# Kernel optimization log

Hardware: AMD Instinct MI355X
Metric: run time of the kernel (lower is better)

## Reference

```python
import jax, jax.numpy as jnp
import numpy as np

S, B, I, H = 512, 256, 256, 256


def setup_inputs() -> dict:
    key = jax.random.key(0)
    ks = jax.random.split(key, 8)
    sc = 0.1
    inputs = jax.random.normal(ks[0], (S, B, I), dtype=jnp.float32)
    h0 = jax.random.normal(ks[1], (1, B, H), dtype=jnp.float32)
    c0 = jax.random.normal(ks[2], (1, B, H), dtype=jnp.float32)
    done = jax.random.randint(ks[3], (S, B), 0, 2).astype(jnp.float32)
    W_ih = jax.random.normal(ks[4], (4 * H, I), dtype=jnp.float32) * sc
    W_hh = jax.random.normal(ks[5], (4 * H, H), dtype=jnp.float32) * sc
    b_ih = jax.random.normal(ks[6], (4 * H,), dtype=jnp.float32) * sc
    b_hh = jax.random.normal(ks[7], (4 * H,), dtype=jnp.float32) * sc
    return {"inputs": inputs, "h0": h0, "c0": c0, "done": done,
            "W_ih": W_ih, "W_hh": W_hh, "b_ih": b_ih, "b_hh": b_hh}


def _lstm_with_dones(inputs, h0, c0, done, W_ih, W_hh, b_ih, b_hh):
    Hd = h0.shape[-1]
    bias = b_ih + b_hh  # (4H,)
    # Precompute input projections for all timesteps: (S, B, 4H)
    x_proj = jnp.einsum('sbi,gi->sbg', inputs, W_ih) + bias

    def step(carry, xs):
        h, c = carry                      # (B, H) each
        xp, d = xs                        # (B, 4H), (B,)
        mask = (1.0 - d)[:, None]         # reset state where done
        h = h * mask
        c = c * mask
        gates = xp + h @ W_hh.T           # (B, 4H), torch gate order i,f,g,o
        i_g, f_g, g_g, o_g = jnp.split(gates, 4, axis=-1)
        c = jax.nn.sigmoid(f_g) * c + jax.nn.sigmoid(i_g) * jnp.tanh(g_g)
        h = jax.nn.sigmoid(o_g) * jnp.tanh(c)
        return (h, c), h

    (hT, cT), hs = jax.lax.scan(step, (h0[0], c0[0]), (x_proj, done))
    new_hidden = hs.reshape(-1, Hd)       # flatten (S, B, H) -> (S*B, H)
    return new_hidden, hT[None], cT[None]


def reference(inputs, h0, c0, done, W_ih, W_hh, b_ih, b_hh):
    return _lstm_with_dones(inputs, h0, c0, done, W_ih, W_hh, b_ih, b_hh)
```

## Files before the change

### kernel.cpp

```cpp
#include <hip/hip_runtime.h>
#include <hip/hip_bf16.h>

typedef unsigned int u32;
typedef unsigned short u16;
typedef __attribute__((ext_vector_type(8))) short bf16x8;
typedef __attribute__((ext_vector_type(8))) unsigned short u16x8;
typedef __attribute__((ext_vector_type(4))) float f32x4;
typedef __attribute__((ext_vector_type(4))) float f4;

#define HS_TOTAL 33554432
#define MAXTILES 2048


__device__ __forceinline__ u16 f2bf(float f) {
  u32 u = __builtin_bit_cast(u32, f);
  u += 0x7fffu + ((u >> 16) & 1u);
  return (u16)(u >> 16);
}
__device__ __forceinline__ float sigm(float x) {
  return __builtin_amdgcn_rcpf(1.f + __builtin_amdgcn_exp2f(-1.44269504088896f * x));
}
__device__ __forceinline__ float tanh_(float x) {
  return 1.f - 2.f * __builtin_amdgcn_rcpf(1.f + __builtin_amdgcn_exp2f(2.88539008177793f * x));
}

__global__ void k_pack(const float* __restrict__ Wih, const float* __restrict__ Whh,
                       const float* __restrict__ bih, const float* __restrict__ bhh,
                       u16* __restrict__ wpack, float* __restrict__ bias) {
  int blk = blockIdx.x;
  int ln = threadIdx.x;
  if (blk >= 1024) {
    int g = (blk - 1024) * 64 + ln;
    bias[g] = bih[g] + bhh[g];
    return;
  }
  const float* W = (blk >> 9) ? Whh : Wih;
  int nt = (blk >> 3) & 63, kt = blk & 7;
  int g = nt * 16 + (ln & 15);
  int kb = kt * 32 + (ln >> 4) * 8;
  const float* src = W + g * 256 + kb;
  u16x8 v;
#pragma unroll
  for (int j = 0; j < 8; j++) v[j] = f2bf(src[j]);
  *(u16x8*)(wpack + (size_t)blk * 512 + ln * 8) = v;
}

__global__ void k_segscan(const float* __restrict__ done, u32* __restrict__ cnt,
                          u32* __restrict__ hist, u32* __restrict__ segs) {
  __shared__ float ld[512][5];
  __shared__ u32 lhist[513];
  int t = threadIdx.x;
  for (int i = t; i < 513; i += 256) lhist[i] = 0;
  int b0 = blockIdx.x * 4;
  for (int s = t; s < 512; s += 256) {
    f4 v = *(const f4*)(done + s * 256 + b0);
    ld[s][0] = v[0]; ld[s][1] = v[1]; ld[s][2] = v[2]; ld[s][3] = v[3];
  }
  __syncthreads();
  int wv = t >> 6, ln = t & 63;
  int b = b0 + wv;
  u32 myrec[8];
  int mycnt = 0;
  for (int j = 0; j < 8; j++) {
    int s = ln * 8 + j;
    float d = ld[s][wv];
    bool bnd = (s == 0) || (d != 0.f);
    if (bnd) {
      int s2 = s + 1;
      while (s2 < 512 && ld[s2][wv] == 0.f) s2++;
      u32 len = (u32)(s2 - s);
      u32 h0f = (s == 0 && d == 0.f) ? 1u : 0u;
      myrec[mycnt++] = (u32)b | ((u32)s << 8) | (len << 17) | (h0f << 27);
    }
  }
  u32 incl = (u32)mycnt;
  for (int d = 1; d < 64; d <<= 1) {
    u32 o = (u32)__shfl_up((int)incl, d);
    if (ln >= d) incl += o;
  }
  u32 total = (u32)__shfl((int)incl, 63);
  u32 base = 0;
  if (ln == 0) base = atomicAdd(cnt, total);
  base = (u32)__shfl((int)base, 0);
  u32 off = base + incl - (u32)mycnt;
  for (int i = 0; i < mycnt; i++) {
    segs[off + i] = myrec[i];
    atomicAdd(&lhist[(myrec[i] >> 17) & 1023], 1u);
  }
  __syncthreads();
  for (int i = t; i < 513; i += 256)
    if (lhist[i]) atomicAdd(&hist[i], lhist[i]);
}

__global__ void k_prefix(const u32* __restrict__ hist, u32* __restrict__ offs) {
  __shared__ u32 h[513];
  int t = threadIdx.x;
  if (t < 513) h[t] = hist[t];
  __syncthreads();
  if (t < 513) {
    u32 s = 0;
    for (int l = t + 1; l < 513; l++) s += h[l];
    offs[t] = s;
  }
}

__global__ void k_scatter(const u32* __restrict__ cnt, const u32* __restrict__ segs,
                          u32* __restrict__ offs, u32* __restrict__ sorted) {
  __shared__ u32 lh[513];
  __shared__ u32 gb[513];
  int t = threadIdx.x;
  for (int i = t; i < 513; i += 512) lh[i] = 0;
  __syncthreads();
  u32 n = *cnt;
  u32 i = blockIdx.x * 512 + t;
  u32 rec = 0, lpos = 0;
  bool v = (i < n);
  if (v) {
    rec = segs[i];
    lpos = atomicAdd(&lh[(rec >> 17) & 1023], 1u);
  }
  __syncthreads();
  for (int j = t; j < 513; j += 512) gb[j] = lh[j] ? atomicAdd(&offs[j], lh[j]) : 0u;
  __syncthreads();
  if (v) sorted[gb[(rec >> 17) & 1023] + lpos] = rec;
}

__global__ __launch_bounds__(512, 2) void k_main(
    const float* __restrict__ inp, const float* __restrict__ h0,
    const float* __restrict__ c0, const u16* __restrict__ wpack,
    const float* __restrict__ bias, const u32* __restrict__ cnt,
    const u32* __restrict__ sorted, float* __restrict__ out) {
  __shared__ __align__(16) u16 Ax[64 * 256];
  __shared__ __align__(16) u16 Ah[64 * 256];
  __shared__ float Cs[64 * 257];
  __shared__ u32 meta[64];
  __shared__ int s_h0;

  u32 nseg = *cnt;
  u32 base = blockIdx.x * 64u;
  if (base >= nseg) return;
  int tid = threadIdx.x;
  if (tid == 0) s_h0 = 0;
  __syncthreads();
  if (tid < 64) {
    u32 i = base + (u32)tid;
    u32 rec = (i < nseg) ? sorted[i] : 0u;
    meta[tid] = rec;
    if ((rec >> 27) & 1u) s_h0 = 1;
  }
  __syncthreads();

  const int maxlen = (int)((meta[0] >> 17) & 1023u);
  const int has0 = s_h0;
  const int w = tid >> 6, lane = tid & 63;
  const int srow = tid >> 3, scg = tid & 7;
  const u32 srec = meta[srow];
  const int s_len = (int)((srec >> 17) & 1023u);
  const int s_b = (int)(srec & 255u);
  const int s_st = (int)((srec >> 8) & 511u);
  char* AxB = (char*)&Ax[0];
  char* AhB = (char*)&Ah[0];
  const int swzS = (srow & 7) << 4;
  const int l15 = lane & 15, lhi = lane >> 4;
  const int lhi16 = lhi << 4;
  const int aswz = (lane & 7) << 4;

  {
    bool hh = ((srec >> 27) & 1u) != 0u;
    const f4* hp = (const f4*)(h0 + s_b * 256 + scg * 32);
#pragma unroll
    for (int u = 0; u < 4; u++) {
      u16x8 v = (u16x8){0, 0, 0, 0, 0, 0, 0, 0};
      if (hh) {
        f4 a0 = hp[2 * u], a1 = hp[2 * u + 1];
        v = (u16x8){f2bf(a0[0]), f2bf(a0[1]), f2bf(a0[2]), f2bf(a0[3]),
                    f2bf(a1[0]), f2bf(a1[1]), f2bf(a1[2]), f2bf(a1[3])};
      }
      *(u16x8*)(AhB + srow * 512 + ((scg * 64 + u * 16) ^ swzS)) = v;
    }
  }
  if (s_len > 0) {
    const f4* p = (const f4*)(inp + ((size_t)(s_st * 256 + s_b)) * 256 + scg * 32);
#pragma unroll
    for (int u = 0; u < 4; u++) {
      f4 x0 = __builtin_nontemporal_load(p + 2 * u);
      f4 x1 = __builtin_nontemporal_load(p + 2 * u + 1);
      u16x8 v = (u16x8){f2bf(x0[0]), f2bf(x0[1]), f2bf(x0[2]), f2bf(x0[3]),
                        f2bf(x1[0]), f2bf(x1[1]), f2bf(x1[2]), f2bf(x1[3])};
      *(u16x8*)(AxB + srow * 512 + ((scg * 64 + u * 16) ^ swzS)) = v;
    }
  } else {
    u16x8 z = (u16x8){0, 0, 0, 0, 0, 0, 0, 0};
#pragma unroll
    for (int u = 0; u < 4; u++)
      *(u16x8*)(AxB + srow * 512 + ((scg * 64 + u * 16) ^ swzS)) = z;
  }
  for (int i = tid; i < 16384; i += 512) {
    int m = i >> 8, j = i & 255;
    u32 rr = meta[m];
    Cs[m * 257 + j] = ((rr >> 27) & 1u) ? c0[(rr & 255u) * 256 + j] : 0.f;
  }
  float bias_r[4][2];
#pragma unroll
  for (int q = 0; q < 4; q++)
#pragma unroll
    for (int t2 = 0; t2 < 2; t2++)
      bias_r[q][t2] = bias[q * 256 + w * 32 + t2 * 16 + l15];
  __syncthreads();

  const u16* wl = wpack + lane * 8 + w * 8192;

  for (int r = 0; r < maxlen; r++) {
    f32x4 acc[4][4][2];
#pragma unroll
    for (int mt = 0; mt < 4; mt++)
#pragma unroll
      for (int q = 0; q < 4; q++)
#pragma unroll
        for (int t2 = 0; t2 < 2; t2++) {
          float bv = bias_r[q][t2];
          acc[mt][q][t2] = (f32x4){bv, bv, bv, bv};
        }

#pragma unroll 1
    for (int kt = 0; kt < 8; kt++) {
      bf16x8 a[4];
#pragma unroll
      for (int mt = 0; mt < 4; mt++)
        a[mt] = *(const bf16x8*)(AxB + (mt * 16 + l15) * 512 + ((kt * 64 + lhi16) ^ aswz));
#pragma unroll
      for (int q = 0; q < 4; q++)
#pragma unroll
        for (int t2 = 0; t2 < 2; t2++) {
          bf16x8 bq = *(const bf16x8*)(wl + q * 65536 + t2 * 4096 + kt * 512);
#pragma unroll
          for (int mt = 0; mt < 4; mt++)
            acc[mt][q][t2] =
                __builtin_amdgcn_mfma_f32_16x16x32_bf16(a[mt], bq, acc[mt][q][t2], 0, 0, 0);
        }
    }
    if (r > 0 || has0) {
#pragma unroll 1
      for (int kt = 0; kt < 8; kt++) {
        bf16x8 a[4];
#pragma unroll
        for (int mt = 0; mt < 4; mt++)
          a[mt] = *(const bf16x8*)(AhB + (mt * 16 + l15) * 512 + ((kt * 64 + lhi16) ^ aswz));
#pragma unroll
        for (int q = 0; q < 4; q++)
#pragma unroll
          for (int t2 = 0; t2 < 2; t2++) {
            bf16x8 bq = *(const bf16x8*)(wl + 262144 + q * 65536 + t2 * 4096 + kt * 512);
#pragma unroll
            for (int mt = 0; mt < 4; mt++)
              acc[mt][q][t2] =
                  __builtin_amdgcn_mfma_f32_16x16x32_bf16(a[mt], bq, acc[mt][q][t2], 0, 0, 0);
          }
      }
    }
    __syncthreads();

    bool stg = (r + 1 < s_len);
    f4 x[8];
    if (stg) {
      const f4* p = (const f4*)(inp + ((size_t)((s_st + r + 1) * 256 + s_b)) * 256 + scg * 32);
#pragma unroll
      for (int u = 0; u < 8; u++) x[u] = __builtin_nontemporal_load(p + u);
    }

#pragma unroll
    for (int mt = 0; mt < 4; mt++)
#pragma unroll
      for (int reg = 0; reg < 4; reg++) {
        int m = mt * 16 + lhi * 4 + reg;
        u32 rr = meta[m];
        int len = (int)((rr >> 17) & 1023u);
        if (r < len) {
          int bb = (int)(rr & 255u);
          int s = (int)((rr >> 8) & 511u) + r;
#pragma unroll
          for (int t2 = 0; t2 < 2; t2++) {
            int j = w * 32 + t2 * 16 + l15;
            float iv = acc[mt][0][t2][reg];
            float fv = acc[mt][1][t2][reg];
            float gv = acc[mt][2][t2][reg];
            float ov = acc[mt][3][t2][reg];
            float cp = Cs[m * 257 + j];
            float cn = sigm(fv) * cp + sigm(iv) * tanh_(gv);
            float hn = sigm(ov) * tanh_(cn);
            Cs[m * 257 + j] = cn;
            __builtin_nontemporal_store(hn, out + ((size_t)(s * 256 + bb)) * 256 + j);
            *((u16*)(AhB + m * 512 + ((2 * j) ^ ((m & 7) << 4)))) = f2bf(hn);
            if (s == 511) {
              out[HS_TOTAL + bb * 256 + j] = hn;
              out[HS_TOTAL + 65536 + bb * 256 + j] = cn;
            }
          }
        }
      }

    if (stg) {
#pragma unroll
      for (int u = 0; u < 4; u++) {
        f4 x0 = x[2 * u], x1 = x[2 * u + 1];
        u16x8 v = (u16x8){f2bf(x0[0]), f2bf(x0[1]), f2bf(x0[2]), f2bf(x0[3]),
                          f2bf(x1[0]), f2bf(x1[1]), f2bf(x1[2]), f2bf(x1[3])};
        *(u16x8*)(AxB + srow * 512 + ((scg * 64 + u * 16) ^ swzS)) = v;
      }
    }
    __syncthreads();
  }
}

extern "C" void kernel_launch(void* const* d_in, const int* in_sizes, int n_in,
                              void* d_out, int out_size, void* d_ws, size_t ws_size,
                              hipStream_t stream) {
  const float* inp = (const float*)d_in[0];
  const float* h0 = (const float*)d_in[1];
  const float* c0 = (const float*)d_in[2];
  const float* done = (const float*)d_in[3];
  const float* Wih = (const float*)d_in[4];
  const float* Whh = (const float*)d_in[5];
  const float* bih = (const float*)d_in[6];
  const float* bhh = (const float*)d_in[7];
  float* out = (float*)d_out;

  char* W = (char*)d_ws;
  u32* cnt = (u32*)W;
  u32* hist = (u32*)(W + 4096);
  u32* offs = (u32*)(W + 8192);
  float* bias = (float*)(W + 16384);
  u16* wpack = (u16*)(W + (1 << 20));
  u32* segs = (u32*)(W + (2 << 20));
  u32* sorted = (u32*)(W + (2 << 20) + (1 << 19));

  hipMemsetAsync(d_ws, 0, 8192, stream);
  k_pack<<<1040, 64, 0, stream>>>(Wih, Whh, bih, bhh, wpack, bias);
  k_segscan<<<64, 256, 0, stream>>>(done, cnt, hist, segs);
  k_prefix<<<1, 1024, 0, stream>>>(hist, offs);
  k_scatter<<<256, 512, 0, stream>>>(cnt, segs, offs, sorted);
  k_main<<<MAXTILES, 512, 0, stream>>>(inp, h0, c0, wpack, bias, cnt, sorted, out);
}
```

Before: 631.6 us.

## Pre-convert inputs to bf16 and stage x via async global-to-LDS loads

Adds a conversion kernel that writes the input sequence as bf16 into the workspace. The main kernel then stages each timestep's x rows straight into LDS with global_load_lds, which halves the per-step input bytes and removes the register round trip and conversion. It also interleaves the packed Wih/Whh layout so one K loop of 16 steps covers both projections, double-buffers the weight fragment loads, and swizzles the cell-state LDS array. The extra conversion pass reads and writes the whole input once more, and the new path only runs when the workspace is large enough, otherwise the old kernel is used.

```diff
diff --git a/kernel.cpp b/kernel.cpp
--- a/kernel.cpp
+++ b/kernel.cpp
@@ -22,6 +22,16 @@
 }
 __device__ __forceinline__ float tanh_(float x) {
   return 1.f - 2.f * __builtin_amdgcn_rcpf(1.f + __builtin_amdgcn_exp2f(2.88539008177793f * x));
+}
+
+__global__ void k_conv(const float* __restrict__ in, u16* __restrict__ outb) {
+  size_t i = ((size_t)blockIdx.x * 256 + threadIdx.x) * 8;
+  const f4* p = (const f4*)(in + i);
+  f4 x0 = __builtin_nontemporal_load(p);
+  f4 x1 = __builtin_nontemporal_load(p + 1);
+  u16x8 v = (u16x8){f2bf(x0[0]), f2bf(x0[1]), f2bf(x0[2]), f2bf(x0[3]),
+                    f2bf(x1[0]), f2bf(x1[1]), f2bf(x1[2]), f2bf(x1[3])};
+  *(u16x8*)(outb + i) = v;
 }
 
 __global__ void k_pack(const float* __restrict__ Wih, const float* __restrict__ Whh,
@@ -34,10 +44,10 @@
     bias[g] = bih[g] + bhh[g];
     return;
   }
-  const float* W = (blk >> 9) ? Whh : Wih;
-  int nt = (blk >> 3) & 63, kt = blk & 7;
+  int nt = blk >> 4, ktm = blk & 15;
+  const float* W = (ktm >> 3) ? Whh : Wih;
   int g = nt * 16 + (ln & 15);
-  int kb = kt * 32 + (ln >> 4) * 8;
+  int kb = (ktm & 7) * 32 + (ln >> 4) * 8;
   const float* src = W + g * 256 + kb;
   u16x8 v;
 #pragma unroll
@@ -126,6 +136,177 @@
 }
 
 __global__ __launch_bounds__(512, 2) void k_main(
+    const u16* __restrict__ inp_bf, const float* __restrict__ h0,
+    const float* __restrict__ c0, const u16* __restrict__ wpack,
+    const float* __restrict__ bias, const u32* __restrict__ cnt,
+    const u32* __restrict__ sorted, float* __restrict__ out) {
+  __shared__ __align__(16) u16 As[2][64][256];
+  __shared__ __align__(16) float Cs[64 * 256];
+  __shared__ u32 meta[64];
+  __shared__ int s_h0;
+
+  u32 nseg = *cnt;
+  u32 base = blockIdx.x * 64u;
+  if (base >= nseg) return;
+  int tid = threadIdx.x;
+  if (tid == 0) s_h0 = 0;
+  __syncthreads();
+  if (tid < 64) {
+    u32 i = base + (u32)tid;
+    u32 rec = (i < nseg) ? sorted[i] : 0u;
+    meta[tid] = rec;
+    if ((rec >> 27) & 1u) s_h0 = 1;
+  }
+  __syncthreads();
+
+  const int maxlen = (int)((meta[0] >> 17) & 1023u);
+  const int has0 = s_h0;
+  const int w = tid >> 6, lane = tid & 63;
+  const int l15 = lane & 15, lhi = lane >> 4;
+  const int srow = tid >> 3, scg = tid & 7;
+  const u32 srec = meta[srow];
+  char* AsB = (char*)&As[0][0][0];
+  char* CsB = (char*)&Cs[0];
+  const int swzS = (srow & 7) << 4;
+
+  {
+    bool hh = ((srec >> 27) & 1u) != 0u;
+    const f4* hp = (const f4*)(h0 + (srec & 255u) * 256 + scg * 32);
+#pragma unroll
+    for (int u = 0; u < 4; u++) {
+      u16x8 v = (u16x8){0, 0, 0, 0, 0, 0, 0, 0};
+      if (hh) {
+        f4 a0 = hp[2 * u], a1 = hp[2 * u + 1];
+        v = (u16x8){f2bf(a0[0]), f2bf(a0[1]), f2bf(a0[2]), f2bf(a0[3]),
+                    f2bf(a1[0]), f2bf(a1[1]), f2bf(a1[2]), f2bf(a1[3])};
+      }
+      *(u16x8*)(AsB + 32768 + srow * 512 + ((scg * 64 + u * 16) ^ swzS)) = v;
+    }
+  }
+  for (int i = tid; i < 16384; i += 512) {
+    int m = i >> 8, j = i & 255;
+    u32 rr = meta[m];
+    float cv = ((rr >> 27) & 1u) ? c0[(rr & 255u) * 256 + j] : 0.f;
+    *(float*)(CsB + m * 1024 + ((4 * j) ^ ((m & 7) << 4))) = cv;
+  }
+  float bias_r[4][2];
+#pragma unroll
+  for (int q = 0; q < 4; q++)
+#pragma unroll
+    for (int t2 = 0; t2 < 2; t2++)
+      bias_r[q][t2] = bias[q * 256 + w * 32 + t2 * 16 + l15];
+
+  const int strow0 = w * 8;
+  const int sl31 = lane & 31;
+  auto stage_x = [&](int r1) {
+#pragma unroll
+    for (int i = 0; i < 4; i++) {
+      int row = strow0 + 2 * i + (lane >> 5);
+      u32 rr = meta[row];
+      int len = (int)((rr >> 17) & 1023u);
+      u16* ldst = &As[0][strow0 + 2 * i][0];
+      if (r1 < len) {
+        int bb = (int)(rr & 255u);
+        int st = (int)((rr >> 8) & 511u);
+        int srcoff = (sl31 * 16) ^ ((row & 7) << 4);
+        const char* src =
+            (const char*)(inp_bf + ((size_t)((st + r1) * 256 + bb)) * 256) + srcoff;
+        __builtin_amdgcn_global_load_lds(
+            (const __attribute__((address_space(1))) void*)src,
+            (__attribute__((address_space(3))) void*)ldst, 16, 0, 0);
+      }
+    }
+  };
+  stage_x(0);
+  __syncthreads();
+
+  const u16* wl = wpack + w * 16384 + lane * 8;
+
+  f32x4 acc[4][4][2];
+  bf16x8 wA[8], wB[8], afr[4];
+
+  auto ldw = [&](bf16x8(&dst)[8], int ktm) {
+#pragma unroll
+    for (int f = 0; f < 8; f++)
+      dst[f] = *(const bf16x8*)(wl + (f >> 1) * 131072 + (f & 1) * 8192 + ktm * 512);
+  };
+  auto lda = [&](int ktm) {
+#pragma unroll
+    for (int mt = 0; mt < 4; mt++) {
+      int row = mt * 16 + l15;
+      afr[mt] = *(const bf16x8*)(AsB + (ktm >> 3) * 32768 + row * 512 +
+                                 (((ktm & 7) * 64 + lhi * 16) ^ ((row & 7) << 4)));
+    }
+  };
+  auto domfma = [&](bf16x8(&wv)[8]) {
+#pragma unroll
+    for (int f = 0; f < 8; f++)
+#pragma unroll
+      for (int mt = 0; mt < 4; mt++)
+        acc[mt][f >> 1][f & 1] =
+            __builtin_amdgcn_mfma_f32_16x16x32_bf16(afr[mt], wv[f], acc[mt][f >> 1][f & 1], 0, 0, 0);
+  };
+
+  for (int r = 0; r < maxlen; r++) {
+#pragma unroll
+    for (int mt = 0; mt < 4; mt++)
+#pragma unroll
+      for (int q = 0; q < 4; q++)
+#pragma unroll
+        for (int t2 = 0; t2 < 2; t2++) {
+          float bv = bias_r[q][t2];
+          acc[mt][q][t2] = (f32x4){bv, bv, bv, bv};
+        }
+
+    const int ktlim = (r > 0 || has0) ? 16 : 8;
+    ldw(wA, 0);
+    for (int kt = 0; kt < ktlim; kt += 2) {
+      ldw(wB, kt + 1);
+      lda(kt);
+      domfma(wA);
+      if (kt + 2 < ktlim) ldw(wA, kt + 2);
+      lda(kt + 1);
+      domfma(wB);
+    }
+    __syncthreads();
+
+    stage_x(r + 1);
+
+#pragma unroll
+    for (int mt = 0; mt < 4; mt++)
+#pragma unroll
+      for (int reg = 0; reg < 4; reg++) {
+        int m = mt * 16 + lhi * 4 + reg;
+        u32 rr = meta[m];
+        int len = (int)((rr >> 17) & 1023u);
+        if (r < len) {
+          int bb = (int)(rr & 255u);
+          int s = (int)((rr >> 8) & 511u) + r;
+#pragma unroll
+          for (int t2 = 0; t2 < 2; t2++) {
+            int j = w * 32 + t2 * 16 + l15;
+            float iv = acc[mt][0][t2][reg];
+            float fv = acc[mt][1][t2][reg];
+            float gv = acc[mt][2][t2][reg];
+            float ov = acc[mt][3][t2][reg];
+            float* cp = (float*)(CsB + m * 1024 + ((4 * j) ^ ((m & 7) << 4)));
+            float cn = sigm(fv) * (*cp) + sigm(iv) * tanh_(gv);
+            float hn = sigm(ov) * tanh_(cn);
+            *cp = cn;
+            __builtin_nontemporal_store(hn, out + ((size_t)(s * 256 + bb)) * 256 + j);
+            *((u16*)(AsB + 32768 + m * 512 + ((2 * j) ^ ((m & 7) << 4)))) = f2bf(hn);
+            if (s == 511) {
+              out[HS_TOTAL + bb * 256 + j] = hn;
+              out[HS_TOTAL + 65536 + bb * 256 + j] = cn;
+            }
+          }
+        }
+      }
+    __syncthreads();
+  }
+}
+
+__global__ __launch_bounds__(512, 2) void k_main_small(
     const float* __restrict__ inp, const float* __restrict__ h0,
     const float* __restrict__ c0, const u16* __restrict__ wpack,
     const float* __restrict__ bias, const u32* __restrict__ cnt,
@@ -208,7 +389,7 @@
       bias_r[q][t2] = bias[q * 256 + w * 32 + t2 * 16 + l15];
   __syncthreads();
 
-  const u16* wl = wpack + lane * 8 + w * 8192;
+  const u16* wl = wpack + w * 16384 + lane * 8;
 
   for (int r = 0; r < maxlen; r++) {
     f32x4 acc[4][4][2];
@@ -232,7 +413,7 @@
       for (int q = 0; q < 4; q++)
 #pragma unroll
         for (int t2 = 0; t2 < 2; t2++) {
-          bf16x8 bq = *(const bf16x8*)(wl + q * 65536 + t2 * 4096 + kt * 512);
+          bf16x8 bq = *(const bf16x8*)(wl + q * 131072 + t2 * 8192 + kt * 512);
 #pragma unroll
           for (int mt = 0; mt < 4; mt++)
             acc[mt][q][t2] =
@@ -250,7 +431,7 @@
         for (int q = 0; q < 4; q++)
 #pragma unroll
           for (int t2 = 0; t2 < 2; t2++) {
-            bf16x8 bq = *(const bf16x8*)(wl + 262144 + q * 65536 + t2 * 4096 + kt * 512);
+            bf16x8 bq = *(const bf16x8*)(wl + q * 131072 + t2 * 8192 + (kt + 8) * 512);
 #pragma unroll
             for (int mt = 0; mt < 4; mt++)
               acc[mt][q][t2] =
@@ -333,11 +514,19 @@
   u16* wpack = (u16*)(W + (1 << 20));
   u32* segs = (u32*)(W + (2 << 20));
   u32* sorted = (u32*)(W + (2 << 20) + (1 << 19));
+  u16* inp_bf = (u16*)(W + (4 << 20));
+
+  const bool big = ws_size >= (size_t)(4 + 65) * 1024 * 1024;
 
   hipMemsetAsync(d_ws, 0, 8192, stream);
   k_pack<<<1040, 64, 0, stream>>>(Wih, Whh, bih, bhh, wpack, bias);
   k_segscan<<<64, 256, 0, stream>>>(done, cnt, hist, segs);
   k_prefix<<<1, 1024, 0, stream>>>(hist, offs);
   k_scatter<<<256, 512, 0, stream>>>(cnt, segs, offs, sorted);
-  k_main<<<MAXTILES, 512, 0, stream>>>(inp, h0, c0, wpack, bias, cnt, sorted, out);
-}
+  if (big) {
+    k_conv<<<16384, 256, 0, stream>>>(inp, inp_bf);
+    k_main<<<MAXTILES, 512, 0, stream>>>(inp_bf, h0, c0, wpack, bias, cnt, sorted, out);
+  } else {
+    k_main_small<<<MAXTILES, 512, 0, stream>>>(inp, h0, c0, wpack, bias, cnt, sorted, out);
+  }
+}
```

Result: faster. 607.4 us (-3.8%).
